# Kernel tuning notes

Measured on AMD Instinct MI355X. Metric: run time of the kernel, lower is better.

Reference implementation:

```python
import jax, jax.numpy as jnp
import numpy as np

B, S, IN, ACT, D, H, TOPK = 512, 128, 64, 8, 256, 4, 8
DH = D // H  # head dim


def setup_inputs() -> dict:
    key = jax.random.key(0)
    ks = jax.random.split(key, 16)
    w = lambda k, shp: jax.random.normal(k, shp, dtype=jnp.float32) * 0.05
    return {
        "prev_d": jax.random.normal(ks[0], (B, D), dtype=jnp.float32),
        "x_obs": jax.random.normal(ks[1], (B, S, IN), dtype=jnp.float32),
        "a_prev": jax.random.normal(ks[2], (B, S, ACT), dtype=jnp.float32),
        # f_x2phi: Linear(IN->D) -> Tanh -> Linear(D -> D-ACT)
        "W1": w(ks[3], (IN, D)), "b1": w(ks[4], (D,)),
        "W2": w(ks[5], (D, D - ACT)), "b2": w(ks[6], (D - ACT,)),
        # transformer (single MHA layer): fused qkv + output proj
        "Wqkv": w(ks[7], (D, 3 * D)), "bqkv": w(ks[8], (3 * D,)),
        "Wo": w(ks[9], (D, D)), "bo": w(ks[10], (D,)),
        # GRUCell(TOPK*D -> D), torch layout transposed to (in, 3*D)
        "W_ih": w(ks[11], (TOPK * D, 3 * D)), "b_ih": w(ks[12], (3 * D,)),
        "W_hh": w(ks[13], (D, 3 * D)), "b_hh": w(ks[14], (3 * D,)),
    }


def _forward(prev_d, x_obs, a_prev, W1, b1, W2, b2, Wqkv, bqkv, Wo, bo,
             W_ih, b_ih, W_hh, b_hh):
    # f_x2phi MLP
    x_phi = jnp.tanh(x_obs @ W1 + b1) @ W2 + b2            # [B,S,D-ACT]
    xa = jnp.concatenate([x_phi, a_prev], axis=-1)          # [B,S,D]
    # single-layer multi-head self-attention (trans_model_q)
    qkv = xa @ Wqkv + bqkv                                  # [B,S,3D]
    q, k, v = jnp.split(qkv, 3, axis=-1)
    q = q.reshape(B, S, H, DH)
    k = k.reshape(B, S, H, DH)
    v = v.reshape(B, S, H, DH)
    scores = jnp.einsum("bqhd,bkhd->bhqk", q, k) / jnp.sqrt(jnp.float32(DH))
    attn = jax.nn.softmax(scores, axis=-1)                  # [B,H,S,S]
    ctx = jnp.einsum("bhqk,bkhd->bqhd", attn, v).reshape(B, S, D)
    trans_out = ctx @ Wo + bo                               # [B,S,D]
    # attention_matrix_align: [H*B,S,S] split by B, cat dim 2 -> [B,S,H*S];
    # sum over last dim == sum over heads and keys of the per-row scores.
    score_sum = scores.sum(axis=(1, 3))                     # [B,S]
    _, idx = jax.lax.top_k(score_sum, TOPK)                 # [B,TOPK] int32
    sel = jnp.take_along_axis(trans_out, idx[:, :, None], axis=1)  # [B,TOPK,D]
    reshaped = sel.reshape(B, TOPK * D)
    # torch GRUCell update
    gi = reshaped @ W_ih + b_ih                             # [B,3D]
    gh = prev_d @ W_hh + b_hh                               # [B,3D]
    i_r, i_z, i_n = jnp.split(gi, 3, axis=-1)
    h_r, h_z, h_n = jnp.split(gh, 3, axis=-1)
    r = jax.nn.sigmoid(i_r + h_r)
    z = jax.nn.sigmoid(i_z + h_z)
    n = jnp.tanh(i_n + r * h_n)
    new_d = (1.0 - z) * n + z * prev_d                      # [B,D]
    return new_d, reshaped


def reference(prev_d, x_obs, a_prev, W1, b1, W2, b2, Wqkv, bqkv, Wo, bo,
              W_ih, b_ih, W_hh, b_hh):
    return _forward(prev_d, x_obs, a_prev, W1, b1, W2, b2, Wqkv, bqkv, Wo, bo,
                    W_ih, b_ih, W_hh, b_hh)
```

## Files before the change

kernel.cpp:

```cpp
#include <hip/hip_runtime.h>
#include <hip/hip_bf16.h>
#include <math.h>

#define BB 512
#define SS 128
#define DD 256
#define HH 4
#define TOPK 8
#define D3 768
#define DMA 248
#define ACT_ 8
#define NTOK 65536

typedef __attribute__((ext_vector_type(8))) short bf16x8;
typedef __attribute__((ext_vector_type(4))) short short4v;
typedef __attribute__((ext_vector_type(4))) float f32x4;

static __device__ __forceinline__ short f2bf(float x) {
    __hip_bfloat16 h = __float2bfloat16(x);
    return *reinterpret_cast<short*>(&h);
}
static __device__ __forceinline__ float bf2f(short s) {
    __hip_bfloat16 h = *reinterpret_cast<__hip_bfloat16*>(&s);
    return __bfloat162float(h);
}
static __device__ __forceinline__ float tanh_fast(float x) {
    float e = __expf(2.f * x);
    return 1.f - 2.f / (e + 1.f);
}

#define HSW(r, c) ((r) * 256 + ((c) ^ (((r) & 7) << 3)))

__device__ __forceinline__ void dev_wsplit(float (*t)[33], const float* src,
        short* dhi, short* dlo, int R, int C, int Cpad, int blk, int tid) {
    const int ctiles = Cpad >> 5;
    const int rt = blk / ctiles, ct = blk % ctiles;
    const int r0 = rt * 32, c0 = ct * 32;
#pragma unroll
    for (int i = 0; i < 4; ++i) {
        int idx = i * 256 + tid;
        int lr = idx >> 5, lc = idx & 31;
        t[lr][lc] = (c0 + lc < C) ? src[(size_t)(r0 + lr) * C + c0 + lc] : 0.f;
    }
    __syncthreads();
#pragma unroll
    for (int i = 0; i < 4; ++i) {
        int idx = i * 256 + tid;
        int lc = idx >> 5, lr = idx & 31;
        float v = t[lr][lc];
        short h = f2bf(v);
        size_t o = (size_t)(c0 + lc) * R + r0 + lr;
        dhi[o] = h;
        dlo[o] = f2bf(v - bf2f(h));
    }
}

__device__ __forceinline__ void dev_trbf(float (*t)[33], const float* src,
        __hip_bfloat16* dst, int R, int C, int blk, int tid) {
    const int ctiles = C >> 5;
    const int rt = blk / ctiles, ct = blk % ctiles;
    const int r0 = rt * 32, c0 = ct * 32;
#pragma unroll
    for (int i = 0; i < 4; ++i) {
        int idx = i * 256 + tid;
        int lr = idx >> 5, lc = idx & 31;
        t[lr][lc] = src[(size_t)(r0 + lr) * C + c0 + lc];
    }
    __syncthreads();
#pragma unroll
    for (int i = 0; i < 4; ++i) {
        int idx = i * 256 + tid;
        int lc = idx >> 5, lr = idx & 31;
        dst[(size_t)(c0 + lc) * R + r0 + lr] = __float2bfloat16(t[lr][lc]);
    }
}

__device__ __forceinline__ void dev_prep(float (*t)[33], const float* Wqkv,
        float* WqT, short* WqTbf, __hip_bfloat16* WkvT, int blk, int tid) {
    const int rt = blk / 24, ct = blk % 24;
    const int r0 = rt * 32, c0 = ct * 32;
#pragma unroll
    for (int i = 0; i < 4; ++i) {
        int idx = i * 256 + tid;
        int lr = idx >> 5, lc = idx & 31;
        t[lr][lc] = Wqkv[(size_t)(r0 + lr) * D3 + c0 + lc];
    }
    __syncthreads();
#pragma unroll
    for (int i = 0; i < 4; ++i) {
        int idx = i * 256 + tid;
        int lc = idx >> 5, lr = idx & 31;
        float v = t[lr][lc];
        int c = c0 + lc, r = r0 + lr;
        if (c < 256) {
            WqT[(size_t)c * 256 + r] = v;
            WqTbf[(size_t)c * 256 + r] = f2bf(v);
        } else {
            WkvT[(size_t)(c - 256) * 256 + r] = __float2bfloat16(v);
        }
    }
}

__global__ void __launch_bounds__(256) k_prepall(
        const float* __restrict__ W1, short* __restrict__ W1Thi, short* __restrict__ W1Tlo,
        const float* __restrict__ W2, short* __restrict__ W2Thi, short* __restrict__ W2Tlo,
        const float* __restrict__ Wqkv, float* __restrict__ WqT, short* __restrict__ WqTbf,
        __hip_bfloat16* __restrict__ WkvT,
        const float* __restrict__ W_ih, __hip_bfloat16* __restrict__ WihT,
        const float* __restrict__ W_hh, __hip_bfloat16* __restrict__ WhhT,
        const float* __restrict__ Wo, __hip_bfloat16* __restrict__ WoT,
        const float* __restrict__ prev_d, __hip_bfloat16* __restrict__ pdbf) {
    __shared__ float t[32][33];
    const int blk = blockIdx.x, tid = threadIdx.x;
    if (blk < 16)        dev_wsplit(t, W1, W1Thi, W1Tlo, 64, 256, 256, blk, tid);
    else if (blk < 80)   dev_wsplit(t, W2, W2Thi, W2Tlo, 256, DMA, 256, blk - 16, tid);
    else if (blk < 272)  dev_prep(t, Wqkv, WqT, WqTbf, WkvT, blk - 80, tid);
    else if (blk < 1808) dev_trbf(t, W_ih, WihT, 2048, 768, blk - 272, tid);
    else if (blk < 2000) dev_trbf(t, W_hh, WhhT, 256, 768, blk - 1808, tid);
    else if (blk < 2064) dev_trbf(t, Wo, WoT, 256, 256, blk - 2000, tid);
    else {
        int i = (blk - 2064) * 1024 + tid * 4;
        float4 v = *(const float4*)&prev_d[i];
        pdbf[i]     = __float2bfloat16(v.x);
        pdbf[i + 1] = __float2bfloat16(v.y);
        pdbf[i + 2] = __float2bfloat16(v.z);
        pdbf[i + 3] = __float2bfloat16(v.w);
    }
}

__global__ void __launch_bounds__(512, 4) k_mlp(const float* __restrict__ x_obs,
        const short* __restrict__ W1Thi, const short* __restrict__ W1Tlo,
        const float* __restrict__ b1,
        const short* __restrict__ W2Thi, const short* __restrict__ W2Tlo,
        const float* __restrict__ b2, const float* __restrict__ a_prev,
        const short* __restrict__ WkvT, const float* __restrict__ bqkv,
        float* __restrict__ xa,
        __hip_bfloat16* __restrict__ kbf, __hip_bfloat16* __restrict__ vbfT) {
    __shared__ __attribute__((aligned(16))) short Hhi[64 * 256];
    __shared__ __attribute__((aligned(16))) short Hlo[64 * 256];
    const int m0 = blockIdx.x * 64;
    const int b = blockIdx.x >> 1;
    const int tb0 = (blockIdx.x & 1) * 64;
    const int tid = threadIdx.x;
    const int wave = tid >> 6, lane = tid & 63;
    const int quad = lane >> 4, l15 = lane & 15;
    const int n0 = wave * 32;

    {
        bf16x8 Bh[2][2], Bl[2][2];
#pragma unroll
        for (int nt = 0; nt < 2; ++nt)
#pragma unroll
            for (int ks = 0; ks < 2; ++ks) {
                size_t o = (size_t)(n0 + nt * 16 + l15) * 64 + ks * 32 + quad * 8;
                Bh[nt][ks] = *(const bf16x8*)&W1Thi[o];
                Bl[nt][ks] = *(const bf16x8*)&W1Tlo[o];
            }
        f32x4 acc[4][2];
#pragma unroll
        for (int mt = 0; mt < 4; ++mt)
#pragma unroll
            for (int nt = 0; nt < 2; ++nt) acc[mt][nt] = (f32x4){0.f, 0.f, 0.f, 0.f};
#pragma unroll
        for (int mt = 0; mt < 4; ++mt) {
            bf16x8 Ah[2], Al[2];
#pragma unroll
            for (int ks = 0; ks < 2; ++ks) {
                const float* xp = &x_obs[(size_t)(m0 + mt * 16 + l15) * 64 + ks * 32 + quad * 8];
                float4 a0 = *(const float4*)xp;
                float4 a1 = *(const float4*)(xp + 4);
                bf16x8 h, l;
                h[0]=f2bf(a0.x); l[0]=f2bf(a0.x - bf2f(h[0]));
                h[1]=f2bf(a0.y); l[1]=f2bf(a0.y - bf2f(h[1]));
                h[2]=f2bf(a0.z); l[2]=f2bf(a0.z - bf2f(h[2]));
                h[3]=f2bf(a0.w); l[3]=f2bf(a0.w - bf2f(h[3]));
                h[4]=f2bf(a1.x); l[4]=f2bf(a1.x - bf2f(h[4]));
                h[5]=f2bf(a1.y); l[5]=f2bf(a1.y - bf2f(h[5]));
                h[6]=f2bf(a1.z); l[6]=f2bf(a1.z - bf2f(h[6]));
                h[7]=f2bf(a1.w); l[7]=f2bf(a1.w - bf2f(h[7]));
                Ah[ks] = h; Al[ks] = l;
            }
#pragma unroll
            for (int nt = 0; nt < 2; ++nt)
#pragma unroll
                for (int ks = 0; ks < 2; ++ks) {
                    acc[mt][nt] = __builtin_amdgcn_mfma_f32_16x16x32_bf16(Ah[ks], Bh[nt][ks], acc[mt][nt], 0, 0, 0);
                    acc[mt][nt] = __builtin_amdgcn_mfma_f32_16x16x32_bf16(Ah[ks], Bl[nt][ks], acc[mt][nt], 0, 0, 0);
                    acc[mt][nt] = __builtin_amdgcn_mfma_f32_16x16x32_bf16(Al[ks], Bh[nt][ks], acc[mt][nt], 0, 0, 0);
                }
        }
#pragma unroll
        for (int nt = 0; nt < 2; ++nt) {
            int col = n0 + nt * 16 + l15;
            float bias = b1[col];
#pragma unroll
            for (int mt = 0; mt < 4; ++mt)
#pragma unroll
                for (int r = 0; r < 4; ++r) {
                    int tl = mt * 16 + quad * 4 + r;
                    float tv = tanh_fast(acc[mt][nt][r] + bias);
                    short h = f2bf(tv);
                    Hhi[HSW(tl, col)] = h;
                    Hlo[HSW(tl, col)] = f2bf(tv - bf2f(h));
                }
        }
    }

    f32x4 acc[4][2];
#pragma unroll
    for (int mt = 0; mt < 4; ++mt)
#pragma unroll
        for (int nt = 0; nt < 2; ++nt) acc[mt][nt] = (f32x4){0.f, 0.f, 0.f, 0.f};

    bf16x8 Bh[2][2], Bl[2][2];
#pragma unroll
    for (int nt = 0; nt < 2; ++nt) {
        size_t o = (size_t)(n0 + nt * 16 + l15) * 256 + quad * 8;
        Bh[0][nt] = *(const bf16x8*)&W2Thi[o];
        Bl[0][nt] = *(const bf16x8*)&W2Tlo[o];
    }
    __syncthreads();

#pragma unroll
    for (int ki = 0; ki < 8; ++ki) {
        const int cur = ki & 1, nxt = cur ^ 1;
        if (ki < 7) {
            int k0n = (ki + 1) * 32;
#pragma unroll
            for (int nt = 0; nt < 2; ++nt) {
                size_t o = (size_t)(n0 + nt * 16 + l15) * 256 + k0n + quad * 8;
                Bh[nxt][nt] = *(const bf16x8*)&W2Thi[o];
                Bl[nxt][nt] = *(const bf16x8*)&W2Tlo[o];
            }
        }
        const int k0 = ki * 32;
#pragma unroll
        for (int mt = 0; mt < 4; ++mt) {
            bf16x8 Ah = *(bf16x8*)&Hhi[HSW(mt * 16 + l15, k0 + quad * 8)];
            bf16x8 Al = *(bf16x8*)&Hlo[HSW(mt * 16 + l15, k0 + quad * 8)];
#pragma unroll
            for (int nt = 0; nt < 2; ++nt) {
                acc[mt][nt] = __builtin_amdgcn_mfma_f32_16x16x32_bf16(Ah, Bh[cur][nt], acc[mt][nt], 0, 0, 0);
                acc[mt][nt] = __builtin_amdgcn_mfma_f32_16x16x32_bf16(Ah, Bl[cur][nt], acc[mt][nt], 0, 0, 0);
                acc[mt][nt] = __builtin_amdgcn_mfma_f32_16x16x32_bf16(Al, Bh[cur][nt], acc[mt][nt], 0, 0, 0);
            }
        }
    }

    __syncthreads();
    short* Xbf = Hhi;
#pragma unroll
    for (int nt = 0; nt < 2; ++nt) {
        int col = n0 + nt * 16 + l15;
        float bias = (col < DMA) ? b2[col] : 0.f;
#pragma unroll
        for (int mt = 0; mt < 4; ++mt)
#pragma unroll
            for (int r = 0; r < 4; ++r) {
                int tl = mt * 16 + quad * 4 + r;
                int token = m0 + tl;
                float v;
                if (col < DMA) v = acc[mt][nt][r] + bias;
                else           v = a_prev[(size_t)token * ACT_ + (col - DMA)];
                xa[(size_t)token * 256 + col] = v;
                Xbf[HSW(tl, col)] = f2bf(v);
            }
    }

    bf16x8 bfv[4][2];
#pragma unroll
    for (int k8 = 0; k8 < 4; ++k8)
#pragma unroll
        for (int nf = 0; nf < 2; ++nf)
            bfv[k8][nf] = *(const bf16x8*)&WkvT[(size_t)(n0 + nf * 16 + l15) * 256
                                                + k8 * 32 + quad * 8];
    __syncthreads();

    for (int ntile = 0; ntile < 2; ++ntile) {
        const int nbase = ntile * 256 + n0;
        f32x4 acc3[4][2];
#pragma unroll
        for (int nf = 0; nf < 2; ++nf) {
            float bias = bqkv[256 + nbase + nf * 16 + l15];
#pragma unroll
            for (int mt = 0; mt < 4; ++mt)
                acc3[mt][nf] = (f32x4){bias, bias, bias, bias};
        }
#pragma unroll
        for (int k8 = 0; k8 < 4; ++k8) {
            const int k0 = k8 * 32;
            bf16x8 af[4];
#pragma unroll
            for (int mt = 0; mt < 4; ++mt)
                af[mt] = *(bf16x8*)&Xbf[HSW(mt * 16 + l15, k0 + quad * 8)];
#pragma unroll
            for (int mt = 0; mt < 4; ++mt)
#pragma unroll
                for (int nf = 0; nf < 2; ++nf)
                    acc3[mt][nf] = __builtin_amdgcn_mfma_f32_16x16x32_bf16(
                        af[mt], bfv[k8][nf], acc3[mt][nf], 0, 0, 0);
        }
#pragma unroll
        for (int k8 = 0; k8 < 4; ++k8)
#pragma unroll
            for (int nf = 0; nf < 2; ++nf)
                bfv[k8][nf] = *(const bf16x8*)&WkvT[(size_t)(nbase + nf * 16 + l15) * 256
                                                    + 128 + k8 * 32 + quad * 8];
#pragma unroll
        for (int k8 = 0; k8 < 4; ++k8) {
            const int k0 = 128 + k8 * 32;
            bf16x8 af[4];
#pragma unroll
            for (int mt = 0; mt < 4; ++mt)
                af[mt] = *(bf16x8*)&Xbf[HSW(mt * 16 + l15, k0 + quad * 8)];
#pragma unroll
            for (int mt = 0; mt < 4; ++mt)
#pragma unroll
                for (int nf = 0; nf < 2; ++nf)
                    acc3[mt][nf] = __builtin_amdgcn_mfma_f32_16x16x32_bf16(
                        af[mt], bfv[k8][nf], acc3[mt][nf], 0, 0, 0);
        }
        if (ntile < 1) {
            const int nb2 = 256 + n0;
#pragma unroll
            for (int k8 = 0; k8 < 4; ++k8)
#pragma unroll
                for (int nf = 0; nf < 2; ++nf)
                    bfv[k8][nf] = *(const bf16x8*)&WkvT[(size_t)(nb2 + nf * 16 + l15) * 256
                                                        + k8 * 32 + quad * 8];
        }
#pragma unroll
        for (int nf = 0; nf < 2; ++nf) {
            int n_g = nbase + nf * 16 + l15;
            if (n_g < 256) {
#pragma unroll
                for (int mt = 0; mt < 4; ++mt)
#pragma unroll
                    for (int r = 0; r < 4; ++r) {
                        int token = tb0 + mt * 16 + quad * 4 + r;
                        kbf[((size_t)b * SS + token) * 256 + n_g] = __float2bfloat16(acc3[mt][nf][r]);
                    }
            } else {
#pragma unroll
                for (int mt = 0; mt < 4; ++mt) {
                    short4v pv;
#pragma unroll
                    for (int r = 0; r < 4; ++r) pv[r] = f2bf(acc3[mt][nf][r]);
                    *(short4v*)((short*)vbfT + ((size_t)b * 256 + (n_g - 256)) * SS
                                + tb0 + mt * 16 + quad * 4) = pv;
                }
            }
        }
    }
}

__global__ void __launch_bounds__(256) k_score(const float* __restrict__ xa,
        const float* __restrict__ Wqkv, const float* __restrict__ WqT,
        const float* __restrict__ bqkv, int* __restrict__ idxb) {
    __shared__ float xasum_sh[256];
    __shared__ float ksum_sh[256];
    __shared__ float wqk_sh[256];
    __shared__ double ssd[128];
    const int b = blockIdx.x;
    const int tid = threadIdx.x;
    const float* xab = xa + (size_t)b * SS * DD;

    float s = 0.f;
    for (int r = 0; r < 128; ++r) s += xab[r * 256 + tid];
    xasum_sh[tid] = s;
    __syncthreads();

    float ks = 128.f * bqkv[256 + tid];
    for (int d = 0; d < 256; ++d)
        ks = fmaf(xasum_sh[d], Wqkv[(size_t)d * D3 + 256 + tid], ks);
    ksum_sh[tid] = ks;
    __syncthreads();

    float wq = 0.f;
    for (int c = 0; c < 256; ++c)
        wq = fmaf(WqT[(size_t)c * 256 + tid], ksum_sh[c], wq);
    wqk_sh[tid] = wq;
    double bqdot = 0.0;
    for (int c = 0; c < 256; ++c)
        bqdot += (double)bqkv[c] * (double)ksum_sh[c];
    __syncthreads();

    {
        const int wv = tid >> 6, lane = tid & 63;
#pragma unroll 4
        for (int rr = 0; rr < 32; ++rr) {
            int r = wv * 32 + rr;
            float4 x4 = *(const float4*)&xab[(size_t)r * 256 + lane * 4];
            const float* w4 = wqk_sh + lane * 4;
            double p = (double)x4.x * (double)w4[0];
            p += (double)x4.y * (double)w4[1];
            p += (double)x4.z * (double)w4[2];
            p += (double)x4.w * (double)w4[3];
#pragma unroll
            for (int off = 1; off < 64; off <<= 1) p += __shfl_xor(p, off);
            if (lane == 0) ssd[r] = (p + bqdot) * 0.125;
        }
    }
    __syncthreads();
    if (tid < 64) {
        double v0 = ssd[tid], v1 = ssd[tid + 64];
        int i0 = tid, i1 = tid + 64;
        bool t0 = false, t1 = false;
        for (int t = 0; t < TOPK; ++t) {
            double c0 = t0 ? -1e300 : v0;
            double c1 = t1 ? -1e300 : v1;
            double bvv; int bi;
            if (c1 > c0) { bvv = c1; bi = i1; } else { bvv = c0; bi = i0; }
#pragma unroll
            for (int off = 1; off < 64; off <<= 1) {
                double ov = __shfl_xor(bvv, off);
                int oi = __shfl_xor(bi, off);
                if (ov > bvv || (ov == bvv && oi < bi)) { bvv = ov; bi = oi; }
            }
            if (tid == 0) idxb[b * TOPK + t] = bi;
            if (bi == i0) t0 = true;
            if (bi == i1) t1 = true;
        }
    }
}

__global__ void __launch_bounds__(256) k_attn2(const float* __restrict__ xa,
        const int* __restrict__ idxb, const short* __restrict__ WqTbf,
        const float* __restrict__ bqkv,
        const short* __restrict__ kbf, const short* __restrict__ vbfT,
        short* __restrict__ Ctx) {
    __shared__ __attribute__((aligned(16))) short Xsh[16 * 264];
    __shared__ __attribute__((aligned(16))) short Qsh[16 * 264];
    __shared__ short Pbuf[4][16 * 136];
    __shared__ int sidx[8];
    const int b = blockIdx.x;
    const int tid = threadIdx.x;
    const int h = tid >> 6, lane = tid & 63;
    const int quad = lane >> 4, l15 = lane & 15;

    if (tid < 8) sidx[tid] = idxb[b * TOPK + tid];
    __syncthreads();
#pragma unroll
    for (int t = 0; t < 16; ++t) {
        short v = 0;
        if (t < 8) v = f2bf(xa[((size_t)b * SS + sidx[t]) * 256 + tid]);
        Xsh[t * 264 + tid] = v;
    }
    __syncthreads();

    {
        f32x4 qacc[4];
#pragma unroll
        for (int nt = 0; nt < 4; ++nt) qacc[nt] = (f32x4){0.f, 0.f, 0.f, 0.f};
#pragma unroll
        for (int ki = 0; ki < 8; ++ki) {
            int k0 = ki * 32;
            bf16x8 Ax = *(bf16x8*)&Xsh[l15 * 264 + k0 + quad * 8];
#pragma unroll
            for (int nt = 0; nt < 4; ++nt) {
                int col = h * 64 + nt * 16 + l15;
                bf16x8 Bq = *(const bf16x8*)&WqTbf[(size_t)col * 256 + k0 + quad * 8];
                qacc[nt] = __builtin_amdgcn_mfma_f32_16x16x32_bf16(Ax, Bq, qacc[nt], 0, 0, 0);
            }
        }
#pragma unroll
        for (int nt = 0; nt < 4; ++nt) {
            int col = h * 64 + nt * 16 + l15;
            float bq = bqkv[col];
#pragma unroll
            for (int r = 0; r < 4; ++r)
                Qsh[(quad * 4 + r) * 264 + col] = f2bf(qacc[nt][r] + bq);
        }
    }

    const short* kb = kbf + (size_t)b * SS * 256 + h * 64;
    const short* vb = vbfT + ((size_t)b * 256 + h * 64) * SS;

    bf16x8 aq[2];
#pragma unroll
    for (int ks = 0; ks < 2; ++ks)
        aq[ks] = *(bf16x8*)&Qsh[l15 * 264 + h * 64 + ks * 32 + quad * 8];
    f32x4 sc[8];
#pragma unroll
    for (int nt = 0; nt < 8; ++nt) sc[nt] = (f32x4){0.f, 0.f, 0.f, 0.f};
#pragma unroll
    for (int nt = 0; nt < 8; ++nt)
#pragma unroll
        for (int ks = 0; ks < 2; ++ks) {
            bf16x8 bk = *(const bf16x8*)&kb[(size_t)(nt * 16 + l15) * 256 + ks * 32 + quad * 8];
            sc[nt] = __builtin_amdgcn_mfma_f32_16x16x32_bf16(aq[ks], bk, sc[nt], 0, 0, 0);
        }
#pragma unroll
    for (int r = 0; r < 4; ++r) {
        float m = -3.4e38f;
#pragma unroll
        for (int nt = 0; nt < 8; ++nt) m = fmaxf(m, sc[nt][r]);
        m = fmaxf(m, __shfl_xor(m, 1));
        m = fmaxf(m, __shfl_xor(m, 2));
        m = fmaxf(m, __shfl_xor(m, 4));
        m = fmaxf(m, __shfl_xor(m, 8));
        float s = 0.f;
#pragma unroll
        for (int nt = 0; nt < 8; ++nt) {
            float e = __expf((sc[nt][r] - m) * 0.125f);
            sc[nt][r] = e;
            s += e;
        }
        s += __shfl_xor(s, 1);
        s += __shfl_xor(s, 2);
        s += __shfl_xor(s, 4);
        s += __shfl_xor(s, 8);
        float inv = 1.f / s;
        int row = quad * 4 + r;
#pragma unroll
        for (int nt = 0; nt < 8; ++nt)
            Pbuf[h][row * 136 + nt * 16 + l15] = f2bf(sc[nt][r] * inv);
    }
    __syncthreads();
    bf16x8 ap[4];
#pragma unroll
    for (int ks = 0; ks < 4; ++ks)
        ap[ks] = *(bf16x8*)&Pbuf[h][l15 * 136 + ks * 32 + quad * 8];
    f32x4 ct[4];
#pragma unroll
    for (int nt = 0; nt < 4; ++nt) ct[nt] = (f32x4){0.f, 0.f, 0.f, 0.f};
#pragma unroll
    for (int nt = 0; nt < 4; ++nt)
#pragma unroll
        for (int ks = 0; ks < 4; ++ks) {
            bf16x8 bv = *(const bf16x8*)&vb[(size_t)(nt * 16 + l15) * SS + ks * 32 + quad * 8];
            ct[nt] = __builtin_amdgcn_mfma_f32_16x16x32_bf16(ap[ks], bv, ct[nt], 0, 0, 0);
        }
#pragma unroll
    for (int nt = 0; nt < 4; ++nt)
#pragma unroll
        for (int r = 0; r < 4; ++r)
            Ctx[((size_t)b * 16 + quad * 4 + r) * 256 + h * 64 + nt * 16 + l15] =
                f2bf(ct[nt][r]);
}

__global__ void __launch_bounds__(256) k_omm(const short* __restrict__ A,
        const short* __restrict__ BT, const float* __restrict__ bias,
        float* __restrict__ resh_out, __hip_bfloat16* __restrict__ resh_bf) {
    __shared__ __attribute__((aligned(16))) short Ash[128 * 72];
    __shared__ __attribute__((aligned(16))) short Bsh[128 * 72];
    const int mt = blockIdx.x >> 1, nt2 = blockIdx.x & 1;
    const int m0 = mt * 128, n0 = nt2 * 128;
    const int tid = threadIdx.x;
    const int wave = tid >> 6, lane = tid & 63;
    const int wm = wave >> 1, wn = wave & 1;
    const int quad = lane >> 4, l15 = lane & 15;

    f32x4 acc[4][4];
#pragma unroll
    for (int tm = 0; tm < 4; ++tm)
#pragma unroll
        for (int tn = 0; tn < 4; ++tn) acc[tm][tn] = (f32x4){0.f, 0.f, 0.f, 0.f};

    for (int k0 = 0; k0 < 256; k0 += 64) {
        __syncthreads();
#pragma unroll
        for (int it = 0; it < 4; ++it) {
            int idx = it * 256 + tid;
            int row = idx >> 3, c8 = idx & 7;
            *(uint4*)&Ash[row * 72 + c8 * 8] =
                *(const uint4*)&A[(size_t)(m0 + row) * 256 + k0 + c8 * 8];
            *(uint4*)&Bsh[row * 72 + c8 * 8] =
                *(const uint4*)&BT[(size_t)(n0 + row) * 256 + k0 + c8 * 8];
        }
        __syncthreads();
#pragma unroll
        for (int ks = 0; ks < 2; ++ks) {
            bf16x8 af[4], bfr[4];
#pragma unroll
            for (int t = 0; t < 4; ++t) {
                af[t]  = *(bf16x8*)&Ash[(wm * 64 + t * 16 + l15) * 72 + ks * 32 + quad * 8];
                bfr[t] = *(bf16x8*)&Bsh[(wn * 64 + t * 16 + l15) * 72 + ks * 32 + quad * 8];
            }
#pragma unroll
            for (int tm = 0; tm < 4; ++tm)
#pragma unroll
                for (int tn = 0; tn < 4; ++tn)
                    acc[tm][tn] = __builtin_amdgcn_mfma_f32_16x16x32_bf16(
                        af[tm], bfr[tn], acc[tm][tn], 0, 0, 0);
        }
    }
#pragma unroll
    for (int tm = 0; tm < 4; ++tm)
#pragma unroll
        for (int tn = 0; tn < 4; ++tn) {
            int col = n0 + wn * 64 + tn * 16 + l15;
            float bv = bias[col];
#pragma unroll
            for (int r = 0; r < 4; ++r) {
                int row = m0 + wm * 64 + tm * 16 + quad * 4 + r;
                int bidx = row >> 4, r16 = row & 15;
                if (r16 < 8) {
                    float v = acc[tm][tn][r] + bv;
                    size_t o = (size_t)bidx * 2048 + r16 * 256 + col;
                    resh_out[o] = v;
                    resh_bf[o] = __float2bfloat16(v);
                }
            }
        }
}

__global__ void __launch_bounds__(256) k_gru2(const __hip_bfloat16* __restrict__ resh_bf,
        const __hip_bfloat16* __restrict__ WihT, const __hip_bfloat16* __restrict__ pdbf,
        const __hip_bfloat16* __restrict__ WhhT, float* __restrict__ gip,
        float* __restrict__ gh) {
    __shared__ __attribute__((aligned(16))) short Ash[128 * 72];
    __shared__ __attribute__((aligned(16))) short Bsh[128 * 72];
    int blk = blockIdx.x;
    const __hip_bfloat16 *A, *BT;
    float* C;
    int K, kbeg, kend;
    if (blk < 96) {
        int chunk = blk / 24; blk %= 24;
        A = resh_bf; BT = WihT; C = gip + (size_t)chunk * 512 * 768;
        K = 2048; kbeg = chunk * 512; kend = kbeg + 512;
    } else {
        blk -= 96; A = pdbf; BT = WhhT; C = gh; K = 256; kbeg = 0; kend = 256;
    }
    const int mt = blk / 6, nt = blk % 6;
    const int m0 = mt * 128, n0 = nt * 128;
    const int tid = threadIdx.x;
    const int wave = tid >> 6, lane = tid & 63;
    const int wm = wave >> 1, wn = wave & 1;
    const int quad = lane >> 4, l15 = lane & 15;

    f32x4 acc[4][4];
#pragma unroll
    for (int tm = 0; tm < 4; ++tm)
#pragma unroll
        for (int tn = 0; tn < 4; ++tn)
            acc[tm][tn] = (f32x4){0.f, 0.f, 0.f, 0.f};

    for (int k0 = kbeg; k0 < kend; k0 += 64) {
        __syncthreads();
#pragma unroll
        for (int it = 0; it < 4; ++it) {
            int idx = it * 256 + tid;
            int row = idx >> 3, c8 = idx & 7;
            *(uint4*)&Ash[row * 72 + c8 * 8] =
                *(const uint4*)&A[(size_t)(m0 + row) * K + k0 + c8 * 8];
            *(uint4*)&Bsh[row * 72 + c8 * 8] =
                *(const uint4*)&BT[(size_t)(n0 + row) * K + k0 + c8 * 8];
        }
        __syncthreads();
#pragma unroll
        for (int ks = 0; ks < 2; ++ks) {
            bf16x8 af[4], bfr[4];
#pragma unroll
            for (int t = 0; t < 4; ++t) {
                af[t]  = *(bf16x8*)&Ash[(wm * 64 + t * 16 + l15) * 72 + ks * 32 + quad * 8];
                bfr[t] = *(bf16x8*)&Bsh[(wn * 64 + t * 16 + l15) * 72 + ks * 32 + quad * 8];
            }
#pragma unroll
            for (int tm = 0; tm < 4; ++tm)
#pragma unroll
                for (int tn = 0; tn < 4; ++tn)
                    acc[tm][tn] = __builtin_amdgcn_mfma_f32_16x16x32_bf16(
                        af[tm], bfr[tn], acc[tm][tn], 0, 0, 0);
        }
    }
#pragma unroll
    for (int tm = 0; tm < 4; ++tm)
#pragma unroll
        for (int tn = 0; tn < 4; ++tn) {
            int col = n0 + wn * 64 + tn * 16 + l15;
#pragma unroll
            for (int r = 0; r < 4; ++r) {
                int row = m0 + wm * 64 + tm * 16 + quad * 4 + r;
                C[(size_t)row * 768 + col] = acc[tm][tn][r];
            }
        }
}

__global__ void k_gruact(const float* __restrict__ gip, const float* __restrict__ gh,
                         const float* __restrict__ b_ih, const float* __restrict__ b_hh,
                         const float* __restrict__ prev_d, float* __restrict__ newd) {
    const int b = blockIdx.x, tid = threadIdx.x;
    const size_t SZ = (size_t)512 * 768;
    const float* g0 = gip + (size_t)b * D3;
    const float* ghb = gh + (size_t)b * D3;
    float ir = ((g0[tid] + g0[SZ + tid]) + g0[2 * SZ + tid]) + g0[3 * SZ + tid] + b_ih[tid];
    float iz = ((g0[256 + tid] + g0[SZ + 256 + tid]) + g0[2 * SZ + 256 + tid]) + g0[3 * SZ + 256 + tid] + b_ih[256 + tid];
    float in = ((g0[512 + tid] + g0[SZ + 512 + tid]) + g0[2 * SZ + 512 + tid]) + g0[3 * SZ + 512 + tid] + b_ih[512 + tid];
    float hr = ghb[tid] + b_hh[tid];
    float hz = ghb[256 + tid] + b_hh[256 + tid];
    float hn = ghb[512 + tid] + b_hh[512 + tid];
    float pd = prev_d[(size_t)b * 256 + tid];
    float r = 1.f / (1.f + __expf(-(ir + hr)));
    float z = 1.f / (1.f + __expf(-(iz + hz)));
    float n = tanhf(in + r * hn);
    newd[(size_t)b * 256 + tid] = (1.f - z) * n + z * pd;
}

extern "C" void kernel_launch(void* const* d_in, const int* in_sizes, int n_in,
                              void* d_out, int out_size, void* d_ws, size_t ws_size,
                              hipStream_t stream) {
    const float* prev_d = (const float*)d_in[0];
    const float* x_obs  = (const float*)d_in[1];
    const float* a_prev = (const float*)d_in[2];
    const float* W1     = (const float*)d_in[3];
    const float* b1     = (const float*)d_in[4];
    const float* W2     = (const float*)d_in[5];
    const float* b2     = (const float*)d_in[6];
    const float* Wqkv   = (const float*)d_in[7];
    const float* bqkv   = (const float*)d_in[8];
    const float* Wo     = (const float*)d_in[9];
    const float* bo     = (const float*)d_in[10];
    const float* W_ih   = (const float*)d_in[11];
    const float* b_ih   = (const float*)d_in[12];
    const float* W_hh   = (const float*)d_in[13];
    const float* b_hh   = (const float*)d_in[14];
    float* out = (float*)d_out;

    const size_t NT = (size_t)BB * SS * DD;
    float* xa = (float*)d_ws;
    short* hkv = (short*)(xa + NT);
    __hip_bfloat16* kbf = (__hip_bfloat16*)hkv;
    __hip_bfloat16* vbfT = (__hip_bfloat16*)(hkv + NT);
    char* r2late = (char*)hkv;
    __hip_bfloat16* resh_bf = (__hip_bfloat16*)r2late;
    float* gip = (float*)(r2late + 2359296);
    float* gh  = (float*)(r2late + 2359296 + 6291456);
    short* xsp = hkv + 2 * NT;
    char* late = (char*)xsp;
    __hip_bfloat16* WihT = (__hip_bfloat16*)late;
    __hip_bfloat16* WhhT = (__hip_bfloat16*)(late + 3145728);
    __hip_bfloat16* WoT  = (__hip_bfloat16*)(late + 3538944);
    short* WqTbf = (short*)(late + 3670016);
    short* Ctx   = (short*)(late + 3801088);
    short* fixed = xsp + 2 * (size_t)NTOK * 64;
    short* W1Thi = fixed;
    short* W1Tlo = W1Thi + 16384;
    short* W2Thi = W1Tlo + 16384;
    short* W2Tlo = W2Thi + 65536;
    float* WqT = (float*)(W2Tlo + 65536);
    __hip_bfloat16* WkvT = (__hip_bfloat16*)(WqT + 65536);
    int* idxb = (int*)(WkvT + 131072);
    __hip_bfloat16* pdbf = (__hip_bfloat16*)(idxb + 4096);

    float* newd = out;
    float* resh = out + (size_t)BB * DD;

    k_prepall <<<2192, 256, 0, stream>>>(W1, W1Thi, W1Tlo, W2, W2Thi, W2Tlo,
                                         Wqkv, WqT, WqTbf, WkvT,
                                         W_ih, WihT, W_hh, WhhT, Wo, WoT,
                                         prev_d, pdbf);
    k_mlp     <<<NTOK / 64, 512, 0, stream>>>(x_obs, W1Thi, W1Tlo, b1,
                                              W2Thi, W2Tlo, b2, a_prev,
                                              (const short*)WkvT, bqkv,
                                              xa, kbf, vbfT);
    k_score   <<<BB, 256, 0, stream>>>(xa, Wqkv, WqT, bqkv, idxb);
    k_attn2   <<<BB, 256, 0, stream>>>(xa, idxb, WqTbf, bqkv,
                                       (const short*)kbf, (const short*)vbfT, Ctx);
    k_omm     <<<128, 256, 0, stream>>>(Ctx, (const short*)WoT, bo, resh, resh_bf);
    k_gru2    <<<120, 256, 0, stream>>>(resh_bf, WihT, pdbf, WhhT, gip, gh);
    k_gruact  <<<BB, 256, 0, stream>>>(gip, gh, b_ih, b_hh, prev_d, newd);
}
```

Measured before the change: 312.4 us.

## Fuse top-k scoring, selected-row attention, and output projection into one kernel

```diff
diff --git a/kernel.cpp b/kernel.cpp
--- a/kernel.cpp
+++ b/kernel.cpp
@@ -354,42 +354,48 @@
     }
 }
 
-__global__ void __launch_bounds__(256) k_score(const float* __restrict__ xa,
+__global__ void __launch_bounds__(256) k_sattn(const float* __restrict__ xa,
         const float* __restrict__ Wqkv, const float* __restrict__ WqT,
-        const float* __restrict__ bqkv, int* __restrict__ idxb) {
+        const float* __restrict__ bqkv, const short* __restrict__ WqTbf,
+        const short* __restrict__ kbf, const short* __restrict__ vbfT,
+        const short* __restrict__ WoT, const float* __restrict__ bo,
+        float* __restrict__ resh_out, __hip_bfloat16* __restrict__ resh_bf) {
     __shared__ float xasum_sh[256];
     __shared__ float ksum_sh[256];
     __shared__ float wqk_sh[256];
     __shared__ double ssd[128];
+    __shared__ int sidx[8];
+    __shared__ __attribute__((aligned(16))) short Xsh[16 * 264];
+    __shared__ __attribute__((aligned(16))) short Qsh[16 * 264];
+    __shared__ short Pbuf[4][16 * 136];
+    __shared__ __attribute__((aligned(16))) short Csh[16 * 264];
     const int b = blockIdx.x;
     const int tid = threadIdx.x;
+    const int h = tid >> 6, lane = tid & 63;
+    const int quad = lane >> 4, l15 = lane & 15;
     const float* xab = xa + (size_t)b * SS * DD;
 
-    float s = 0.f;
-    for (int r = 0; r < 128; ++r) s += xab[r * 256 + tid];
-    xasum_sh[tid] = s;
-    __syncthreads();
-
-    float ks = 128.f * bqkv[256 + tid];
-    for (int d = 0; d < 256; ++d)
-        ks = fmaf(xasum_sh[d], Wqkv[(size_t)d * D3 + 256 + tid], ks);
-    ksum_sh[tid] = ks;
-    __syncthreads();
-
-    float wq = 0.f;
-    for (int c = 0; c < 256; ++c)
-        wq = fmaf(WqT[(size_t)c * 256 + tid], ksum_sh[c], wq);
-    wqk_sh[tid] = wq;
-    double bqdot = 0.0;
-    for (int c = 0; c < 256; ++c)
-        bqdot += (double)bqkv[c] * (double)ksum_sh[c];
-    __syncthreads();
-
     {
-        const int wv = tid >> 6, lane = tid & 63;
+        float s = 0.f;
+        for (int r = 0; r < 128; ++r) s += xab[r * 256 + tid];
+        xasum_sh[tid] = s;
+        __syncthreads();
+
+        float ks = 128.f * bqkv[256 + tid];
+        for (int d = 0; d < 256; ++d)
+            ks = fmaf(xasum_sh[d], Wqkv[(size_t)d * D3 + 256 + tid], ks);
+        ksum_sh[tid] = ks;
+        __syncthreads();
+
+        float wq = 0.f;
+        for (int c = 0; c < 256; ++c)
+            wq = fmaf(WqT[(size_t)c * 256 + tid], ksum_sh[c], wq);
+        wqk_sh[tid] = wq;
+        __syncthreads();
+
 #pragma unroll 4
         for (int rr = 0; rr < 32; ++rr) {
-            int r = wv * 32 + rr;
+            int r = h * 32 + rr;
             float4 x4 = *(const float4*)&xab[(size_t)r * 256 + lane * 4];
             const float* w4 = wqk_sh + lane * 4;
             double p = (double)x4.x * (double)w4[0];
@@ -398,48 +404,32 @@
             p += (double)x4.w * (double)w4[3];
 #pragma unroll
             for (int off = 1; off < 64; off <<= 1) p += __shfl_xor(p, off);
-            if (lane == 0) ssd[r] = (p + bqdot) * 0.125;
-        }
-    }
-    __syncthreads();
-    if (tid < 64) {
-        double v0 = ssd[tid], v1 = ssd[tid + 64];
-        int i0 = tid, i1 = tid + 64;
-        bool t0 = false, t1 = false;
-        for (int t = 0; t < TOPK; ++t) {
-            double c0 = t0 ? -1e300 : v0;
-            double c1 = t1 ? -1e300 : v1;
-            double bvv; int bi;
-            if (c1 > c0) { bvv = c1; bi = i1; } else { bvv = c0; bi = i0; }
-#pragma unroll
-            for (int off = 1; off < 64; off <<= 1) {
-                double ov = __shfl_xor(bvv, off);
-                int oi = __shfl_xor(bi, off);
-                if (ov > bvv || (ov == bvv && oi < bi)) { bvv = ov; bi = oi; }
-            }
-            if (tid == 0) idxb[b * TOPK + t] = bi;
-            if (bi == i0) t0 = true;
-            if (bi == i1) t1 = true;
-        }
-    }
-}
-
-__global__ void __launch_bounds__(256) k_attn2(const float* __restrict__ xa,
-        const int* __restrict__ idxb, const short* __restrict__ WqTbf,
-        const float* __restrict__ bqkv,
-        const short* __restrict__ kbf, const short* __restrict__ vbfT,
-        short* __restrict__ Ctx) {
-    __shared__ __attribute__((aligned(16))) short Xsh[16 * 264];
-    __shared__ __attribute__((aligned(16))) short Qsh[16 * 264];
-    __shared__ short Pbuf[4][16 * 136];
-    __shared__ int sidx[8];
-    const int b = blockIdx.x;
-    const int tid = threadIdx.x;
-    const int h = tid >> 6, lane = tid & 63;
-    const int quad = lane >> 4, l15 = lane & 15;
-
-    if (tid < 8) sidx[tid] = idxb[b * TOPK + tid];
-    __syncthreads();
+            if (lane == 0) ssd[r] = p;
+        }
+        __syncthreads();
+        if (tid < 64) {
+            double v0 = ssd[tid], v1 = ssd[tid + 64];
+            int i0 = tid, i1 = tid + 64;
+            bool t0 = false, t1 = false;
+            for (int t = 0; t < TOPK; ++t) {
+                double c0 = t0 ? -1e300 : v0;
+                double c1 = t1 ? -1e300 : v1;
+                double bvv; int bi;
+                if (c1 > c0) { bvv = c1; bi = i1; } else { bvv = c0; bi = i0; }
+#pragma unroll
+                for (int off = 1; off < 64; off <<= 1) {
+                    double ov = __shfl_xor(bvv, off);
+                    int oi = __shfl_xor(bi, off);
+                    if (ov > bvv || (ov == bvv && oi < bi)) { bvv = ov; bi = oi; }
+                }
+                if (tid == 0) sidx[t] = bi;
+                if (bi == i0) t0 = true;
+                if (bi == i1) t1 = true;
+            }
+        }
+        __syncthreads();
+    }
+
 #pragma unroll
     for (int t = 0; t < 16; ++t) {
         short v = 0;
@@ -535,74 +525,39 @@
     for (int nt = 0; nt < 4; ++nt)
 #pragma unroll
         for (int r = 0; r < 4; ++r)
-            Ctx[((size_t)b * 16 + quad * 4 + r) * 256 + h * 64 + nt * 16 + l15] =
-                f2bf(ct[nt][r]);
-}
-
-__global__ void __launch_bounds__(256) k_omm(const short* __restrict__ A,
-        const short* __restrict__ BT, const float* __restrict__ bias,
-        float* __restrict__ resh_out, __hip_bfloat16* __restrict__ resh_bf) {
-    __shared__ __attribute__((aligned(16))) short Ash[128 * 72];
-    __shared__ __attribute__((aligned(16))) short Bsh[128 * 72];
-    const int mt = blockIdx.x >> 1, nt2 = blockIdx.x & 1;
-    const int m0 = mt * 128, n0 = nt2 * 128;
-    const int tid = threadIdx.x;
-    const int wave = tid >> 6, lane = tid & 63;
-    const int wm = wave >> 1, wn = wave & 1;
-    const int quad = lane >> 4, l15 = lane & 15;
-
-    f32x4 acc[4][4];
-#pragma unroll
-    for (int tm = 0; tm < 4; ++tm)
-#pragma unroll
-        for (int tn = 0; tn < 4; ++tn) acc[tm][tn] = (f32x4){0.f, 0.f, 0.f, 0.f};
-
-    for (int k0 = 0; k0 < 256; k0 += 64) {
-        __syncthreads();
-#pragma unroll
-        for (int it = 0; it < 4; ++it) {
-            int idx = it * 256 + tid;
-            int row = idx >> 3, c8 = idx & 7;
-            *(uint4*)&Ash[row * 72 + c8 * 8] =
-                *(const uint4*)&A[(size_t)(m0 + row) * 256 + k0 + c8 * 8];
-            *(uint4*)&Bsh[row * 72 + c8 * 8] =
-                *(const uint4*)&BT[(size_t)(n0 + row) * 256 + k0 + c8 * 8];
-        }
-        __syncthreads();
-#pragma unroll
-        for (int ks = 0; ks < 2; ++ks) {
-            bf16x8 af[4], bfr[4];
-#pragma unroll
-            for (int t = 0; t < 4; ++t) {
-                af[t]  = *(bf16x8*)&Ash[(wm * 64 + t * 16 + l15) * 72 + ks * 32 + quad * 8];
-                bfr[t] = *(bf16x8*)&Bsh[(wn * 64 + t * 16 + l15) * 72 + ks * 32 + quad * 8];
-            }
-#pragma unroll
-            for (int tm = 0; tm < 4; ++tm)
-#pragma unroll
-                for (int tn = 0; tn < 4; ++tn)
-                    acc[tm][tn] = __builtin_amdgcn_mfma_f32_16x16x32_bf16(
-                        af[tm], bfr[tn], acc[tm][tn], 0, 0, 0);
-        }
-    }
-#pragma unroll
-    for (int tm = 0; tm < 4; ++tm)
-#pragma unroll
-        for (int tn = 0; tn < 4; ++tn) {
-            int col = n0 + wn * 64 + tn * 16 + l15;
-            float bv = bias[col];
+            Csh[(quad * 4 + r) * 264 + h * 64 + nt * 16 + l15] = f2bf(ct[nt][r]);
+    __syncthreads();
+
+    {
+        f32x4 oacc[4];
+#pragma unroll
+        for (int nt = 0; nt < 4; ++nt) oacc[nt] = (f32x4){0.f, 0.f, 0.f, 0.f};
+#pragma unroll
+        for (int ki = 0; ki < 8; ++ki) {
+            bf16x8 af = *(bf16x8*)&Csh[l15 * 264 + ki * 32 + quad * 8];
+#pragma unroll
+            for (int nt = 0; nt < 4; ++nt) {
+                int col = h * 64 + nt * 16 + l15;
+                bf16x8 bw = *(const bf16x8*)&WoT[(size_t)col * 256 + ki * 32 + quad * 8];
+                oacc[nt] = __builtin_amdgcn_mfma_f32_16x16x32_bf16(af, bw, oacc[nt], 0, 0, 0);
+            }
+        }
+#pragma unroll
+        for (int nt = 0; nt < 4; ++nt) {
+            int col = h * 64 + nt * 16 + l15;
+            float bv = bo[col];
 #pragma unroll
             for (int r = 0; r < 4; ++r) {
-                int row = m0 + wm * 64 + tm * 16 + quad * 4 + r;
-                int bidx = row >> 4, r16 = row & 15;
-                if (r16 < 8) {
-                    float v = acc[tm][tn][r] + bv;
-                    size_t o = (size_t)bidx * 2048 + r16 * 256 + col;
+                int row = quad * 4 + r;
+                if (row < 8) {
+                    float v = oacc[nt][r] + bv;
+                    size_t o = (size_t)b * 2048 + row * 256 + col;
                     resh_out[o] = v;
                     resh_bf[o] = __float2bfloat16(v);
                 }
             }
         }
+    }
 }
 
 __global__ void __launch_bounds__(256) k_gru2(const __hip_bfloat16* __restrict__ resh_bf,
@@ -723,7 +678,6 @@
     __hip_bfloat16* kbf = (__hip_bfloat16*)hkv;
     __hip_bfloat16* vbfT = (__hip_bfloat16*)(hkv + NT);
     char* r2late = (char*)hkv;
-    __hip_bfloat16* resh_bf = (__hip_bfloat16*)r2late;
     float* gip = (float*)(r2late + 2359296);
     float* gh  = (float*)(r2late + 2359296 + 6291456);
     short* xsp = hkv + 2 * NT;
@@ -732,7 +686,7 @@
     __hip_bfloat16* WhhT = (__hip_bfloat16*)(late + 3145728);
     __hip_bfloat16* WoT  = (__hip_bfloat16*)(late + 3538944);
     short* WqTbf = (short*)(late + 3670016);
-    short* Ctx   = (short*)(late + 3801088);
+    __hip_bfloat16* resh_bf = (__hip_bfloat16*)(late + 3801088);
     short* fixed = xsp + 2 * (size_t)NTOK * 64;
     short* W1Thi = fixed;
     short* W1Tlo = W1Thi + 16384;
@@ -754,10 +708,9 @@
                                               W2Thi, W2Tlo, b2, a_prev,
                                               (const short*)WkvT, bqkv,
                                               xa, kbf, vbfT);
-    k_score   <<<BB, 256, 0, stream>>>(xa, Wqkv, WqT, bqkv, idxb);
-    k_attn2   <<<BB, 256, 0, stream>>>(xa, idxb, WqTbf, bqkv,
-                                       (const short*)kbf, (const short*)vbfT, Ctx);
-    k_omm     <<<128, 256, 0, stream>>>(Ctx, (const short*)WoT, bo, resh, resh_bf);
+    k_sattn   <<<BB, 256, 0, stream>>>(xa, Wqkv, WqT, bqkv, WqTbf,
+                                       (const short*)kbf, (const short*)vbfT,
+                                       (const short*)WoT, bo, resh, resh_bf);
     k_gru2    <<<120, 256, 0, stream>>>(resh_bf, WihT, pdbf, WhhT, gip, gh);
     k_gruact  <<<BB, 256, 0, stream>>>(gip, gh, b_ih, b_hh, prev_d, newd);
 }
```

Measured after the change: 294.9 us. -5.6%, faster.
